# Optimization experiments

Measured on AMD Instinct MI355X. Metric: run time of the kernel, lower is better.

The kernel has to match this reference:

```python
import jax, jax.numpy as jnp
import numpy as np

B, TC, TP = 2, 1024, 512
NVC, NVP = 8, 4
D, K, H, DFF, L, HOR, NQ = 128, 3, 8, 512, 2, 96, 3
DK = D // H
MASK_VAL = -1e4  # finite stand-in for -inf; entmax15 support never reaches entries this far below the row max


def entmax15(z):
    # Exact 1.5-entmax over the last axis (Peters & Martins sort-based algorithm).
    z = z / 2.0
    z = z - jnp.max(z, axis=-1, keepdims=True)
    zs = jnp.flip(jnp.sort(z, axis=-1), axis=-1)  # descending
    kk = jnp.arange(1, z.shape[-1] + 1, dtype=z.dtype)
    mean = jnp.cumsum(zs, axis=-1) / kk
    meansq = jnp.cumsum(zs * zs, axis=-1) / kk
    ss = kk * (meansq - mean * mean)
    delta = (1.0 - ss) / kk
    pos = delta > 0
    sqrt_d = jnp.where(pos, jnp.sqrt(jnp.where(pos, delta, 1.0)), 0.0)  # grad-safe sqrt
    tau = mean - sqrt_d
    support = jnp.sum((tau <= zs).astype(jnp.int32), axis=-1, keepdims=True)
    tau_star = jnp.take_along_axis(tau, support - 1, axis=-1)
    return jnp.square(jnp.clip(z - tau_star, 0.0, None))


def layer_norm(x, g, b, eps=1e-5):
    m = jnp.mean(x, axis=-1, keepdims=True)
    v = jnp.mean(jnp.square(x - m), axis=-1, keepdims=True)
    return (x - m) * jax.lax.rsqrt(v + eps) * g + b


def selector(x, conv_w, conv_b, sel_w, sel_b, key):
    # x: [B, T, nv]; causal depthwise-grouped conv -> per-var local states [B, T, nv, D]
    Bs, T, nv = x.shape
    xc = jnp.transpose(x, (0, 2, 1))  # [B, nv, T]
    out = jax.lax.conv_general_dilated(
        xc, conv_w, window_strides=(1,), padding=[(K - 1, 0)],
        dimension_numbers=('NCH', 'OIH', 'NCH'), feature_group_count=nv)
    ls = out.reshape(Bs, nv, D, T) + conv_b[None, :, :, None]
    ls = jnp.transpose(ls, (0, 3, 1, 2))  # [B, T, nv, D]
    scores = ls @ sel_w + sel_b  # [B, T, nv]
    scores = jnp.clip(scores, -10.0, 10.0)
    scores = scores + 1e-4 * jax.random.normal(key, scores.shape, scores.dtype)
    w = entmax15(scores)  # [B, T, nv]
    weighted = jnp.sum(ls * w[..., None], axis=2)  # [B, T, D]
    return weighted, w


def attn_block(x, Wq, bq, Wk, bk, Wv, bv, Wo, bo):
    Bs, T, _ = x.shape
    q = (x @ Wq + bq).reshape(Bs, T, H, DK)
    k = (x @ Wk + bk).reshape(Bs, T, H, DK)
    v = (x @ Wv + bv).reshape(Bs, T, H, DK)
    scores = jnp.einsum('bthd,bshd->bhts', q, k) / jnp.sqrt(jnp.float32(DK))
    mask = jnp.triu(jnp.ones((T, T), bool), 1)
    scores = jnp.where(mask[None, None], MASK_VAL, scores)
    w = entmax15(scores)            # [B, H, T, T]
    w_avg = jnp.mean(w, axis=1)     # [B, T, T]
    v_comb = jnp.mean(v, axis=2)    # [B, T, DK]
    out = jnp.einsum('bts,bsd->btd', w_avg, v_comb)
    return out @ Wo + bo, w_avg


def forward(x_cond, x_pred, cw_c, cb_c, sw_c, sb_c, cw_p, cb_p, sw_p, sb_p,
            Wq, bq, Wk, bk, Wv, bv, Wo, bo, ln1_g, ln1_b,
            fw1, fb1, fw2, fb2, ln2_g, ln2_b, proj_w, proj_b):
    nk = jax.random.key(42)
    xc, v_cond = selector(x_cond, cw_c, cb_c, sw_c, sb_c, jax.random.fold_in(nk, 0))
    xp, v_pred = selector(x_pred, cw_p, cb_p, sw_p, sb_p, jax.random.fold_in(nk, 1))
    x = jnp.concatenate([xc, xp], axis=1)  # [B, TC+TP, D]
    logs = []
    for l in range(L):
        a, w = attn_block(x, Wq[l], bq[l], Wk[l], bk[l], Wv[l], bv[l], Wo[l], bo[l])
        x = layer_norm(x + a, ln1_g[l], ln1_b[l])
        h = jax.nn.relu(x @ fw1[l] + fb1[l])
        x = layer_norm(h @ fw2[l] + fb2[l] + x, ln2_g[l], ln2_b[l])
        logs.append(w)
    seq_last = x[:, -1, :]
    out = jnp.einsum('bd,qdh->bqh', seq_last, proj_w) + proj_b  # [B, NQ, HOR]
    return out, v_cond, v_pred, jnp.stack(logs)


def setup_inputs():
    key = jax.random.key(0)
    ks = jax.random.split(key, 16)
    def w(i, shp):
        return (0.02 * jax.random.normal(ks[i], shp)).astype(jnp.float32)
    z = lambda shp: jnp.zeros(shp, jnp.float32)
    o = lambda shp: jnp.ones(shp, jnp.float32)
    return {
        'x_cond': jax.random.normal(ks[0], (B, TC, NVC), jnp.float32),
        'x_pred': jax.random.normal(ks[1], (B, TP, NVP), jnp.float32),
        'cw_c': w(2, (NVC * D, 1, K)), 'cb_c': z((NVC, D)),
        'sw_c': w(3, (D,)), 'sb_c': z((1,)),
        'cw_p': w(4, (NVP * D, 1, K)), 'cb_p': z((NVP, D)),
        'sw_p': w(5, (D,)), 'sb_p': z((1,)),
        'Wq': w(6, (L, D, D)), 'bq': z((L, D)),
        'Wk': w(7, (L, D, D)), 'bk': z((L, D)),
        'Wv': w(8, (L, D, D)), 'bv': z((L, D)),
        'Wo': w(9, (L, DK, D)), 'bo': z((L, D)),
        'ln1_g': o((L, D)), 'ln1_b': z((L, D)),
        'fw1': w(10, (L, D, DFF)), 'fb1': z((L, DFF)),
        'fw2': w(11, (L, DFF, D)), 'fb2': z((L, D)),
        'ln2_g': o((L, D)), 'ln2_b': z((L, D)),
        'proj_w': w(12, (NQ, D, HOR)), 'proj_b': z((NQ, HOR)),
    }


def reference(x_cond, x_pred, cw_c, cb_c, sw_c, sb_c, cw_p, cb_p, sw_p, sb_p,
              Wq, bq, Wk, bk, Wv, bv, Wo, bo, ln1_g, ln1_b,
              fw1, fb1, fw2, fb2, ln2_g, ln2_b, proj_w, proj_b):
    return forward(x_cond, x_pred, cw_c, cb_c, sw_c, sb_c, cw_p, cb_p, sw_p, sb_p,
                   Wq, bq, Wk, bk, Wv, bv, Wo, bo, ln1_g, ln1_b,
                   fw1, fb1, fw2, fb2, ln2_g, ln2_b, proj_w, proj_b)
```

## Files before the change

### kernel.cpp

```cpp
#include <hip/hip_runtime.h>

namespace {

constexpr int NB_  = 2;
constexpr int TC_  = 1024;
constexpr int TP_  = 512;
constexpr int TT_  = 1536;
constexpr int D_   = 128;
constexpr int H_   = 8;
constexpr int DK_  = 16;
constexpr int DFF_ = 512;
constexpr int L_   = 2;
constexpr int HOR_ = 96;
constexpr int NQ_  = 3;

constexpr int SCP_ = TT_ + 8;

typedef _Float16 h2 __attribute__((ext_vector_type(2)));

constexpr int OFF_OUT  = 0;
constexpr int OFF_VC   = NB_ * NQ_ * HOR_;
constexpr int OFF_VP   = OFF_VC + NB_ * TC_ * 8;
constexpr int OFF_LOGS = OFF_VP + NB_ * TP_ * 4;

constexpr int WS_XA  = 0;
constexpr int WS_XB  = WS_XA  + NB_ * TT_ * D_;
constexpr int WS_Q16 = WS_XB  + NB_ * TT_ * D_;
constexpr int WS_K16 = WS_Q16 + NB_ * TT_ * D_ / 2;
constexpr int WS_VC  = WS_K16 + NB_ * TT_ * D_ / 2;
constexpr int WS_WVC = WS_VC  + NB_ * TT_ * DK_;
constexpr int WS_BVC = WS_WVC + L_ * D_ * DK_;

__device__ inline unsigned short f2bf(float x) {
    unsigned u = __float_as_uint(x);
    u = (u + 0x7fffu + ((u >> 16) & 1u)) >> 16;
    return (unsigned short)u;
}
__device__ inline float bf2f_lo(unsigned dw) { return __uint_as_float(dw << 16); }
__device__ inline float bf2f_hi(unsigned dw) { return __uint_as_float(dw & 0xffff0000u); }

__device__ inline float dot2f(h2 a, h2 b, float c) {
#if __has_builtin(__builtin_amdgcn_fdot2)
    return __builtin_amdgcn_fdot2(a, b, c, false);
#else
    return c + (float)a[0] * (float)b[0] + (float)a[1] * (float)b[1];
#endif
}

template <int NV>
__device__ inline void selector_body(
    const float* __restrict__ x, const float* __restrict__ cw,
    const float* __restrict__ cb, const float* __restrict__ sw,
    const float* __restrict__ sb, float* __restrict__ vout,
    float* __restrict__ xout, int Tsel, int row_off, int blk)
{
    const int b = blk / Tsel;
    const int t = blk - b * Tsel;
    const int d = threadIdx.x;
    const int lane = d & 63, wave = d >> 6;

    __shared__ float wsum[2][NV];
    __shared__ float wls[NV];

    float xw[3 * NV];
    #pragma unroll
    for (int kk = 0; kk < 3; ++kk) {
        const int ts = t + kk - 2;
        #pragma unroll
        for (int v = 0; v < NV; ++v)
            xw[kk * NV + v] = (ts >= 0) ? x[((long)b * Tsel + ts) * NV + v] : 0.0f;
    }

    float ls[NV];
    #pragma unroll
    for (int v = 0; v < NV; ++v) {
        const float* cwp = cw + ((long)(v * D_ + d)) * 3;
        float a = cb[v * D_ + d];
        a = fmaf(xw[0 * NV + v], cwp[0], a);
        a = fmaf(xw[1 * NV + v], cwp[1], a);
        a = fmaf(xw[2 * NV + v], cwp[2], a);
        ls[v] = a;
    }

    {
        const float swd = sw[d];
        float p[NV];
        #pragma unroll
        for (int v = 0; v < NV; ++v) p[v] = ls[v] * swd;
        #pragma unroll
        for (int off = 32; off; off >>= 1) {
            #pragma unroll
            for (int v = 0; v < NV; ++v) p[v] += __shfl_xor(p[v], off);
        }
        if (lane == 0) {
            #pragma unroll
            for (int v = 0; v < NV; ++v) wsum[wave][v] = p[v];
        }
    }
    __syncthreads();

    if (d == 0) {
        float u[NV];
        float m = -1e30f;
        #pragma unroll
        for (int v = 0; v < NV; ++v) {
            float s = wsum[0][v] + wsum[1][v] + sb[0];
            s = fminf(fmaxf(s, -10.0f), 10.0f);
            u[v] = 0.5f * s;
            m = fmaxf(m, u[v]);
        }
        float tau = m - 1.0f;
        for (int it = 0; it < 40; ++it) {
            float S1 = 0.f, S2 = 0.f;
            #pragma unroll
            for (int v = 0; v < NV; ++v) {
                float dd = fmaxf(u[v] - tau, 0.f);
                S1 += dd; S2 = fmaf(dd, dd, S2);
            }
            const float f = S2 - 1.0f;
            if (f < 1e-7f) break;
            tau += f / (2.0f * S1);
        }
        #pragma unroll
        for (int v = 0; v < NV; ++v) {
            float dd = fmaxf(u[v] - tau, 0.f);
            wls[v] = dd * dd;
        }
    }
    __syncthreads();

    float acc = 0.f;
    #pragma unroll
    for (int v = 0; v < NV; ++v) acc = fmaf(ls[v], wls[v], acc);
    xout[((long)b * TT_ + row_off + t) * D_ + d] = acc;
    if (d < NV) vout[((long)b * Tsel + t) * NV + d] = wls[d];
}

__device__ inline void prep_body(
    const float* __restrict__ Wv, const float* __restrict__ bv,
    float* __restrict__ wvc, float* __restrict__ bvc, int l)
{
    const float* W  = Wv + (long)l * D_ * D_;
    const float* bb = bv + l * D_;
    float* wv = wvc + l * D_ * DK_;
    float* bo = bvc + l * DK_;
    const int tid = threadIdx.x;
    for (int idx = tid; idx < D_ * DK_; idx += 128) {
        const int i = idx >> 4, dk = idx & 15;
        float s = 0.f;
        #pragma unroll
        for (int hh = 0; hh < H_; ++hh) s += W[i * D_ + hh * DK_ + dk];
        wv[idx] = s * 0.125f;
    }
    if (tid < DK_) {
        float s = 0.f;
        #pragma unroll
        for (int hh = 0; hh < H_; ++hh) s += bb[hh * DK_ + tid];
        bo[tid] = s * 0.125f;
    }
}

__global__ __launch_bounds__(128) void pre_kernel(
    const float* __restrict__ x_cond, const float* __restrict__ cw_c,
    const float* __restrict__ cb_c, const float* __restrict__ sw_c,
    const float* __restrict__ sb_c,
    const float* __restrict__ x_pred, const float* __restrict__ cw_p,
    const float* __restrict__ cb_p, const float* __restrict__ sw_p,
    const float* __restrict__ sb_p,
    const float* __restrict__ Wv, const float* __restrict__ bv,
    float* __restrict__ vc_out, float* __restrict__ vp_out,
    float* __restrict__ xout, float* __restrict__ wvc,
    float* __restrict__ bvc)
{
    const int blk = blockIdx.x;
    if (blk < NB_ * TC_) {
        selector_body<8>(x_cond, cw_c, cb_c, sw_c, sb_c, vc_out, xout,
                         TC_, 0, blk);
    } else if (blk < NB_ * TC_ + NB_ * TP_) {
        selector_body<4>(x_pred, cw_p, cb_p, sw_p, sb_p, vp_out, xout,
                         TP_, TC_, blk - NB_ * TC_);
    } else {
        prep_body(Wv, bv, wvc, bvc, blk - (NB_ * TC_ + NB_ * TP_));
    }
}

__global__ __launch_bounds__(256) void qkv_kernel(
    const float* __restrict__ x,
    const float* __restrict__ Wq, const float* __restrict__ bq,
    const float* __restrict__ Wk, const float* __restrict__ bk,
    const float* __restrict__ wvc, const float* __restrict__ bvc,
    _Float16* __restrict__ q16, _Float16* __restrict__ k16,
    float* __restrict__ vc)
{
    __shared__ float xrT[D_][4];
    const long row0 = (long)blockIdx.x * 4;
    const int tid = threadIdx.x;

    for (int idx = tid; idx < 4 * D_; idx += 256) {
        const int r = idx >> 7, i = idx & 127;
        xrT[i][r] = x[row0 * D_ + idx];
    }
    __syncthreads();

    const int c = tid & 127;
    const int which = tid >> 7;
    const float* __restrict__ W = which ? Wk : Wq;
    const float bb = which ? bk[c] : bq[c];
    float a0 = bb, a1 = bb, a2 = bb, a3 = bb;
    for (int i = 0; i < D_; ++i) {
        const float wv = W[i * D_ + c];
        const float4 xv = *(const float4*)&xrT[i][0];
        a0 = fmaf(xv.x, wv, a0);
        a1 = fmaf(xv.y, wv, a1);
        a2 = fmaf(xv.z, wv, a2);
        a3 = fmaf(xv.w, wv, a3);
    }
    _Float16* __restrict__ dst = which ? k16 : q16;
    dst[(row0 + 0) * D_ + c] = (_Float16)a0;
    dst[(row0 + 1) * D_ + c] = (_Float16)a1;
    dst[(row0 + 2) * D_ + c] = (_Float16)a2;
    dst[(row0 + 3) * D_ + c] = (_Float16)a3;

    if (tid < 64) {
        const int r = tid >> 4, c16 = tid & 15;
        float av = bvc[c16];
        for (int i = 0; i < D_; ++i)
            av = fmaf(xrT[i][r], wvc[i * DK_ + c16], av);
        vc[(row0 + r) * DK_ + c16] = av;
    }
}

template <int NJ>
__device__ inline void entmax_head(unsigned short* __restrict__ srow,
                                   int lane, int t)
{
    const unsigned* __restrict__ rp = (const unsigned*)srow;
    unsigned dw[NJ];
    #pragma unroll
    for (int j = 0; j < NJ; ++j) dw[j] = rp[64 * j + lane];
    float v[2 * NJ];
    #pragma unroll
    for (int j = 0; j < NJ; ++j) {
        const int s0 = 128 * j + 2 * lane;
        v[2*j]   = (s0     <= t) ? bf2f_lo(dw[j]) : -1e30f;
        v[2*j+1] = (s0 + 1 <= t) ? bf2f_hi(dw[j]) : -1e30f;
    }

    float m = -1e30f;
    #pragma unroll
    for (int j = 0; j < 2 * NJ; ++j) m = fmaxf(m, v[j]);
    #pragma unroll
    for (int off = 32; off; off >>= 1) m = fmaxf(m, __shfl_xor(m, off));

    float tau = m - 1.0f;
    for (int it = 0; it < 30; ++it) {
        float S1 = 0.f, S2 = 0.f;
        #pragma unroll
        for (int j = 0; j < 2 * NJ; ++j) {
            const float d0 = fmaxf(v[j] - tau, 0.f);
            S1 += d0; S2 = fmaf(d0, d0, S2);
        }
        #pragma unroll
        for (int off = 32; off; off >>= 1) {
            S1 += __shfl_xor(S1, off);
            S2 += __shfl_xor(S2, off);
        }
        const float f = S2 - 1.0f;
        if (f < 1e-6f) break;
        tau += f / (2.0f * S1);
    }
    unsigned* __restrict__ wp = (unsigned*)srow;
    #pragma unroll
    for (int j = 0; j < NJ; ++j) {
        const float d0 = fmaxf(v[2*j]   - tau, 0.f);
        const float d1 = fmaxf(v[2*j+1] - tau, 0.f);
        const unsigned lo = f2bf(d0 * d0);
        const unsigned hi = f2bf(d1 * d1);
        wp[64 * j + lane] = lo | (hi << 16);
    }
    #pragma unroll
    for (int j = NJ; j < 12; ++j) wp[64 * j + lane] = 0;
}

__global__ __launch_bounds__(256) void attn_kernel(
    const _Float16* __restrict__ q16, const _Float16* __restrict__ k16,
    const float* __restrict__ vcomb, const float* __restrict__ xin,
    float* __restrict__ xout,
    const float* __restrict__ Wo, const float* __restrict__ bo,
    const float* __restrict__ lng, const float* __restrict__ lnb,
    float* __restrict__ logs)
{
    __shared__ unsigned short scb[H_ * SCP_];
    __shared__ _Float16 qrow16[D_];
    __shared__ float red[64];
    __shared__ float o16[DK_];
    __shared__ float yrow[D_];
    __shared__ float stat[2];

    const int blk = blockIdx.x;
    const int b = blk / TT_;
    const int t = blk - b * TT_;
    const int tid = threadIdx.x;
    const int lane = tid & 63, wave = tid >> 6;
    const long rowq  = (long)b * TT_ + t;
    const long bbase = (long)b * TT_;

    if (tid < 64)
        ((unsigned*)qrow16)[tid] = ((const unsigned*)(q16 + rowq * D_))[tid];
    __syncthreads();

    {
        const int h  = tid & 7;
        const int sl = tid >> 3;
        unsigned short* __restrict__ srow = scb + h * SCP_;
        h2 qv[8];
        __builtin_memcpy(qv, (const _Float16*)qrow16 + h * DK_, 32);
        for (int s = sl; s <= t; s += 32) {
            float4 kk0, kk1;
            {
                const float4* kp4 = (const float4*)(k16 + (bbase + s) * D_ + h * DK_);
                kk0 = kp4[0]; kk1 = kp4[1];
            }
            h2 kh[8];
            __builtin_memcpy(kh,     &kk0, 16);
            __builtin_memcpy(kh + 4, &kk1, 16);
            float dot = 0.f;
            #pragma unroll
            for (int i2 = 0; i2 < 8; ++i2) dot = dot2f(qv[i2], kh[i2], dot);
            srow[s] = f2bf(dot * 0.125f);
        }
    }
    __syncthreads();

    if (t < 767) {
        for (int hh = 0; hh < 2; ++hh)
            entmax_head<6>(scb + (wave * 2 + hh) * SCP_, lane, t);
    } else {
        for (int hh = 0; hh < 2; ++hh)
            entmax_head<12>(scb + (wave * 2 + hh) * SCP_, lane, t);
    }
    __syncthreads();

    float4 A0 = make_float4(0,0,0,0), A1 = A0, A2 = A0, A3 = A0;
    float* lrow = logs + rowq * TT_;
    const unsigned* __restrict__ rp0 = (const unsigned*)scb;
    #pragma unroll
    for (int it = 0; it < 3; ++it) {
        const int dwi = tid + 256 * it;
        const int s0 = 2 * dwi;
        float wa0 = 0.f, wa1 = 0.f;
        #pragma unroll
        for (int h = 0; h < H_; ++h) {
            const unsigned d = rp0[h * (SCP_ / 2) + dwi];
            wa0 += bf2f_lo(d);
            wa1 += bf2f_hi(d);
        }
        wa0 *= 0.125f; wa1 *= 0.125f;
        if (s0 <= t) {
            const float4* vp = (const float4*)(vcomb + (bbase + s0) * DK_);
            const float4 v0 = vp[0], v1 = vp[1], v2 = vp[2], v3 = vp[3];
            A0.x = fmaf(wa0, v0.x, A0.x); A0.y = fmaf(wa0, v0.y, A0.y);
            A0.z = fmaf(wa0, v0.z, A0.z); A0.w = fmaf(wa0, v0.w, A0.w);
            A1.x = fmaf(wa0, v1.x, A1.x); A1.y = fmaf(wa0, v1.y, A1.y);
            A1.z = fmaf(wa0, v1.z, A1.z); A1.w = fmaf(wa0, v1.w, A1.w);
            A2.x = fmaf(wa0, v2.x, A2.x); A2.y = fmaf(wa0, v2.y, A2.y);
            A2.z = fmaf(wa0, v2.z, A2.z); A2.w = fmaf(wa0, v2.w, A2.w);
            A3.x = fmaf(wa0, v3.x, A3.x); A3.y = fmaf(wa0, v3.y, A3.y);
            A3.z = fmaf(wa0, v3.z, A3.z); A3.w = fmaf(wa0, v3.w, A3.w);
        }
        if (s0 + 1 <= t) {
            const float4* vp = (const float4*)(vcomb + (bbase + s0 + 1) * DK_);
            const float4 v0 = vp[0], v1 = vp[1], v2 = vp[2], v3 = vp[3];
            A0.x = fmaf(wa1, v0.x, A0.x); A0.y = fmaf(wa1, v0.y, A0.y);
            A0.z = fmaf(wa1, v0.z, A0.z); A0.w = fmaf(wa1, v0.w, A0.w);
            A1.x = fmaf(wa1, v1.x, A1.x); A1.y = fmaf(wa1, v1.y, A1.y);
            A1.z = fmaf(wa1, v1.z, A1.z); A1.w = fmaf(wa1, v1.w, A1.w);
            A2.x = fmaf(wa1, v2.x, A2.x); A2.y = fmaf(wa1, v2.y, A2.y);
            A2.z = fmaf(wa1, v2.z, A2.z); A2.w = fmaf(wa1, v2.w, A2.w);
            A3.x = fmaf(wa1, v3.x, A3.x); A3.y = fmaf(wa1, v3.y, A3.y);
            A3.z = fmaf(wa1, v3.z, A3.z); A3.w = fmaf(wa1, v3.w, A3.w);
        }
        *(float2*)(lrow + s0) = make_float2(wa0, wa1);
    }
    #pragma unroll
    for (int off = 32; off; off >>= 1) {
        A0.x += __shfl_xor(A0.x, off); A0.y += __shfl_xor(A0.y, off);
        A0.z += __shfl_xor(A0.z, off); A0.w += __shfl_xor(A0.w, off);
        A1.x += __shfl_xor(A1.x, off); A1.y += __shfl_xor(A1.y, off);
        A1.z += __shfl_xor(A1.z, off); A1.w += __shfl_xor(A1.w, off);
        A2.x += __shfl_xor(A2.x, off); A2.y += __shfl_xor(A2.y, off);
        A2.z += __shfl_xor(A2.z, off); A2.w += __shfl_xor(A2.w, off);
        A3.x += __shfl_xor(A3.x, off); A3.y += __shfl_xor(A3.y, off);
        A3.z += __shfl_xor(A3.z, off); A3.w += __shfl_xor(A3.w, off);
    }
    if (lane == 0) {
        float* r = red + wave * 16;
        r[0]=A0.x; r[1]=A0.y; r[2]=A0.z; r[3]=A0.w;
        r[4]=A1.x; r[5]=A1.y; r[6]=A1.z; r[7]=A1.w;
        r[8]=A2.x; r[9]=A2.y; r[10]=A2.z; r[11]=A2.w;
        r[12]=A3.x; r[13]=A3.y; r[14]=A3.z; r[15]=A3.w;
    }
    __syncthreads();
    if (tid < DK_) o16[tid] = red[tid] + red[16 + tid] + red[32 + tid] + red[48 + tid];
    __syncthreads();

    float y = 0.f;
    if (tid < D_) {
        float a = bo[tid];
        #pragma unroll
        for (int j = 0; j < DK_; ++j) a = fmaf(o16[j], Wo[j * D_ + tid], a);
        y = xin[rowq * D_ + tid] + a;
        yrow[tid] = y;
    }
    __syncthreads();
    if (tid < 64) {
        float sm = yrow[tid] + yrow[tid + 64];
        #pragma unroll
        for (int off = 32; off; off >>= 1) sm += __shfl_xor(sm, off);
        if (tid == 0) stat[0] = sm * (1.0f / D_);
    }
    __syncthreads();
    if (tid < 64) {
        const float mean = stat[0];
        const float d0 = yrow[tid] - mean, d1 = yrow[tid + 64] - mean;
        float sv = fmaf(d0, d0, d1 * d1);
        #pragma unroll
        for (int off = 32; off; off >>= 1) sv += __shfl_xor(sv, off);
        if (tid == 0) stat[1] = sv * (1.0f / D_);
    }
    __syncthreads();
    if (tid < D_) {
        const float r = rsqrtf(stat[1] + 1e-5f);
        xout[rowq * D_ + tid] = (y - stat[0]) * r * lng[tid] + lnb[tid];
    }
}

__global__ __launch_bounds__(256) void ffn_kernel(
    const float* __restrict__ xin, float* __restrict__ xout,
    const float* __restrict__ fw1, const float* __restrict__ fb1,
    const float* __restrict__ fw2, const float* __restrict__ fb2,
    const float* __restrict__ g, const float* __restrict__ bta,
    int do_proj, const float* __restrict__ pw,
    const float* __restrict__ pb, float* __restrict__ outp)
{
    __shared__ float xrT[D_][4];
    __shared__ float hbT[DFF_][4];
    __shared__ float yb[4][D_];
    __shared__ float xn[D_];

    const long row0 = (long)blockIdx.x * 4;
    const int tid = threadIdx.x;

    for (int idx = tid; idx < 4 * D_; idx += 256) {
        const int r = idx >> 7, i = idx & 127;
        xrT[i][r] = xin[row0 * D_ + idx];
    }
    __syncthreads();

    {
        const int c = tid;
        float4 a0 = make_float4(0,0,0,0), a1 = a0;
        for (int i = 0; i < D_; ++i) {
            const float w0 = fw1[i * DFF_ + c];
            const float w1 = fw1[i * DFF_ + c + 256];
            const float4 xv = *(const float4*)&xrT[i][0];
            a0.x = fmaf(xv.x, w0, a0.x); a0.y = fmaf(xv.y, w0, a0.y);
            a0.z = fmaf(xv.z, w0, a0.z); a0.w = fmaf(xv.w, w0, a0.w);
            a1.x = fmaf(xv.x, w1, a1.x); a1.y = fmaf(xv.y, w1, a1.y);
            a1.z = fmaf(xv.z, w1, a1.z); a1.w = fmaf(xv.w, w1, a1.w);
        }
        const float b0 = fb1[c], b1 = fb1[c + 256];
        float4 h0, h1;
        h0.x = fmaxf(a0.x + b0, 0.f); h0.y = fmaxf(a0.y + b0, 0.f);
        h0.z = fmaxf(a0.z + b0, 0.f); h0.w = fmaxf(a0.w + b0, 0.f);
        h1.x = fmaxf(a1.x + b1, 0.f); h1.y = fmaxf(a1.y + b1, 0.f);
        h1.z = fmaxf(a1.z + b1, 0.f); h1.w = fmaxf(a1.w + b1, 0.f);
        *(float4*)&hbT[c][0]       = h0;
        *(float4*)&hbT[c + 256][0] = h1;
    }
    __syncthreads();

    {
        const int d = tid & 127;
        const int r0 = (tid >> 7) * 2;
        float a0 = 0.f, a1 = 0.f;
        for (int j = 0; j < DFF_; ++j) {
            const float wv = fw2[j * D_ + d];
            const float2 hv = *(const float2*)&hbT[j][r0];
            a0 = fmaf(hv.x, wv, a0);
            a1 = fmaf(hv.y, wv, a1);
        }
        const float bb = fb2[d];
        yb[r0 + 0][d] = a0 + bb + xrT[d][r0 + 0];
        yb[r0 + 1][d] = a1 + bb + xrT[d][r0 + 1];
    }
    __syncthreads();

    const int w = tid >> 6, lane = tid & 63;
    const bool pblk = do_proj && (((row0 + 4) % TT_) == 0);
    {
        const float y0 = yb[w][lane], y1 = yb[w][lane + 64];
        float sm = y0 + y1;
        #pragma unroll
        for (int off = 32; off; off >>= 1) sm += __shfl_xor(sm, off);
        const float mean = sm * (1.0f / D_);
        const float d0 = y0 - mean, d1 = y1 - mean;
        float sv = fmaf(d0, d0, d1 * d1);
        #pragma unroll
        for (int off = 32; off; off >>= 1) sv += __shfl_xor(sv, off);
        const float rcp = rsqrtf(sv * (1.0f / D_) + 1e-5f);
        const float o0 = d0 * rcp * g[lane]      + bta[lane];
        const float o1 = d1 * rcp * g[lane + 64] + bta[lane + 64];
        xout[(row0 + w) * D_ + lane]      = o0;
        xout[(row0 + w) * D_ + lane + 64] = o1;
        if (pblk && w == 3) { xn[lane] = o0; xn[lane + 64] = o1; }
    }
    if (pblk) {
        __syncthreads();
        const int b = (int)((row0 + 3) / TT_);
        for (int idx = tid; idx < NQ_ * HOR_; idx += 256) {
            const int qq = idx / HOR_, hh = idx - qq * HOR_;
            float s = pb[idx];
            for (int d = 0; d < D_; ++d)
                s = fmaf(xn[d], pw[((long)qq * D_ + d) * HOR_ + hh], s);
            outp[b * NQ_ * HOR_ + idx] = s;
        }
    }
}

}

extern "C" void kernel_launch(void* const* d_in, const int* in_sizes, int n_in,
                              void* d_out, int out_size, void* d_ws, size_t ws_size,
                              hipStream_t stream) {
    (void)in_sizes; (void)n_in; (void)out_size; (void)ws_size;

    const float* x_cond = (const float*)d_in[0];
    const float* x_pred = (const float*)d_in[1];
    const float* cw_c   = (const float*)d_in[2];
    const float* cb_c   = (const float*)d_in[3];
    const float* sw_c   = (const float*)d_in[4];
    const float* sb_c   = (const float*)d_in[5];
    const float* cw_p   = (const float*)d_in[6];
    const float* cb_p   = (const float*)d_in[7];
    const float* sw_p   = (const float*)d_in[8];
    const float* sb_p   = (const float*)d_in[9];
    const float* Wq     = (const float*)d_in[10];
    const float* bq     = (const float*)d_in[11];
    const float* Wk     = (const float*)d_in[12];
    const float* bk     = (const float*)d_in[13];
    const float* Wv     = (const float*)d_in[14];
    const float* bv     = (const float*)d_in[15];
    const float* Wo     = (const float*)d_in[16];
    const float* bo     = (const float*)d_in[17];
    const float* ln1g   = (const float*)d_in[18];
    const float* ln1b   = (const float*)d_in[19];
    const float* fw1    = (const float*)d_in[20];
    const float* fb1    = (const float*)d_in[21];
    const float* fw2    = (const float*)d_in[22];
    const float* fb2    = (const float*)d_in[23];
    const float* ln2g   = (const float*)d_in[24];
    const float* ln2b   = (const float*)d_in[25];
    const float* pw     = (const float*)d_in[26];
    const float* pb     = (const float*)d_in[27];

    float* outp = (float*)d_out;
    float* ws   = (float*)d_ws;
    float*     xA   = ws + WS_XA;
    float*     xB   = ws + WS_XB;
    _Float16*  q16  = (_Float16*)(ws + WS_Q16);
    _Float16*  k16  = (_Float16*)(ws + WS_K16);
    float*     vcb  = ws + WS_VC;
    float*     wvc  = ws + WS_WVC;
    float*     bvc  = ws + WS_BVC;

    pre_kernel<<<NB_ * TC_ + NB_ * TP_ + L_, 128, 0, stream>>>(
        x_cond, cw_c, cb_c, sw_c, sb_c,
        x_pred, cw_p, cb_p, sw_p, sb_p,
        Wv, bv, outp + OFF_VC, outp + OFF_VP, xA, wvc, bvc);

    for (int l = 0; l < L_; ++l) {
        qkv_kernel<<<NB_ * TT_ / 4, 256, 0, stream>>>(
            xA, Wq + (long)l * D_ * D_, bq + l * D_,
            Wk + (long)l * D_ * D_, bk + l * D_,
            wvc + l * D_ * DK_, bvc + l * DK_, q16, k16, vcb);
        attn_kernel<<<NB_ * TT_, 256, 0, stream>>>(
            q16, k16, vcb, xA, xB,
            Wo + (long)l * DK_ * D_, bo + l * D_,
            ln1g + l * D_, ln1b + l * D_,
            outp + OFF_LOGS + (long)l * NB_ * TT_ * TT_);
        ffn_kernel<<<NB_ * TT_ / 4, 256, 0, stream>>>(
            xB, xA, fw1 + (long)l * D_ * DFF_, fb1 + l * DFF_,
            fw2 + (long)l * DFF_ * D_, fb2 + l * D_,
            ln2g + l * D_, ln2b + l * D_,
            (l == L_ - 1) ? 1 : 0, pw, pb, outp);
    }
}
```

Baseline: 349.1 us.

## Fix Newton iterations for entmax tau with exact support-based finish; reorder attention blocks longest-first

The entmax threshold solve now runs a fixed, unrolled number of Newton steps with no convergence check, then computes tau exactly in closed form from the identified support set (mean minus sqrt). This removes the divergent early-exit loop and its per-iteration branch. The attention kernel's block-to-row mapping is also reversed so the longest causal rows (largest t) are scheduled first, which should improve tail load balance. The risk is wrong output if the fixed step count does not yet identify the correct support.

Measured after the change: 348.1 us. Within noise of the previous version (-0.3%).

```diff
diff --git a/kernel.cpp b/kernel.cpp
--- a/kernel.cpp
+++ b/kernel.cpp
@@ -110,16 +110,24 @@
             m = fmaxf(m, u[v]);
         }
         float tau = m - 1.0f;
-        for (int it = 0; it < 40; ++it) {
+        for (int it = 0; it < 12; ++it) {
             float S1 = 0.f, S2 = 0.f;
             #pragma unroll
             for (int v = 0; v < NV; ++v) {
                 float dd = fmaxf(u[v] - tau, 0.f);
                 S1 += dd; S2 = fmaf(dd, dd, S2);
             }
-            const float f = S2 - 1.0f;
-            if (f < 1e-7f) break;
-            tau += f / (2.0f * S1);
+            tau += (S2 - 1.0f) / (2.0f * S1);
+        }
+        {
+            float S1 = 0.f, S2 = 0.f, K = 0.f;
+            #pragma unroll
+            for (int v = 0; v < NV; ++v) {
+                if (u[v] > tau) { S1 += u[v]; S2 = fmaf(u[v], u[v], S2); K += 1.f; }
+            }
+            const float mean = S1 / K;
+            const float arg  = fmaxf(fmaf(mean, mean, -(S2 - 1.0f) / K), 0.f);
+            tau = mean - sqrtf(arg);
         }
         #pragma unroll
         for (int v = 0; v < NV; ++v) {
@@ -253,7 +261,8 @@
     for (int off = 32; off; off >>= 1) m = fmaxf(m, __shfl_xor(m, off));
 
     float tau = m - 1.0f;
-    for (int it = 0; it < 30; ++it) {
+    #pragma unroll
+    for (int it = 0; it < 7; ++it) {
         float S1 = 0.f, S2 = 0.f;
         #pragma unroll
         for (int j = 0; j < 2 * NJ; ++j) {
@@ -265,9 +274,23 @@
             S1 += __shfl_xor(S1, off);
             S2 += __shfl_xor(S2, off);
         }
-        const float f = S2 - 1.0f;
-        if (f < 1e-6f) break;
-        tau += f / (2.0f * S1);
+        tau += (S2 - 1.0f) / (2.0f * S1);
+    }
+    {
+        float S1 = 0.f, S2 = 0.f, K = 0.f;
+        #pragma unroll
+        for (int j = 0; j < 2 * NJ; ++j) {
+            if (v[j] > tau) { S1 += v[j]; S2 = fmaf(v[j], v[j], S2); K += 1.f; }
+        }
+        #pragma unroll
+        for (int off = 32; off; off >>= 1) {
+            S1 += __shfl_xor(S1, off);
+            S2 += __shfl_xor(S2, off);
+            K  += __shfl_xor(K,  off);
+        }
+        const float mean = S1 / K;
+        const float arg  = fmaxf(fmaf(mean, mean, -(S2 - 1.0f) / K), 0.f);
+        tau = mean - sqrtf(arg);
     }
     unsigned* __restrict__ wp = (unsigned*)srow;
     #pragma unroll
@@ -298,8 +321,8 @@
     __shared__ float stat[2];
 
     const int blk = blockIdx.x;
-    const int b = blk / TT_;
-    const int t = blk - b * TT_;
+    const int t = TT_ - 1 - (blk >> 1);
+    const int b = blk & 1;
     const int tid = threadIdx.x;
     const int lane = tid & 63, wave = tid >> 6;
     const long rowq  = (long)b * TT_ + t;
```
